# Performance work log

Measured on AMD Instinct MI355X. Metric: run time of the kernel, lower is better.

## Reference

```python
import jax, jax.numpy as jnp
import numpy as np

B, N, D, R = 4, 192, 128, 32


def _sh_l1(r):
    # e3nn l=1 real SH with 'integral' normalization: sqrt(3/4pi) * r_hat
    rh = r / (jnp.linalg.norm(r, axis=-1, keepdims=True) + 1e-12)
    return np.sqrt(3.0 / (4.0 * np.pi)).astype(np.float32) * rh


def _sh_l2(r):
    # l=2 real SH of unit vector, integral normalization, standard m=-2..2 order
    rh = r / (jnp.linalg.norm(r, axis=-1, keepdims=True) + 1e-12)
    x, y, z = rh[..., 0], rh[..., 1], rh[..., 2]
    c = np.float32(0.5 / np.sqrt(np.pi))
    s15 = np.float32(np.sqrt(15.0))
    s5h = np.float32(0.5 * np.sqrt(5.0))
    return c * jnp.stack([s15 * x * y, s15 * y * z, s5h * (3.0 * z * z - 1.0),
                          s15 * x * z, 0.5 * s15 * (x * x - y * y)], axis=-1)


def _radial(x, W1, b1, W2, b2):
    return jax.nn.silu(x @ W1 + b1) @ W2 + b2


def _forward(node_s, node_v, node_t, rbf, r_hat, mask,
             Ws1, bs1, Ws2, bs2, Wd1, bd1, Wd2, bd2,
             Wv1, bv1, Wv2, bv2, Wt1, bt1, Wt2, bt2,
             ln_g, ln_b, Wo, bo, v_scale, t_scale):
    m = mask[..., None]                      # (B,N,N,1)
    Y1 = _sh_l1(r_hat)                       # (B,N,N,3)
    Y2 = _sh_l2(r_hat)                       # (B,N,N,5)
    # scalar messages: h_j[b,i,j,d] = node_s[b,j,d]*mask; w0 also masked (mask applied twice, as in source)
    w0 = _radial(rbf, Ws1, bs1, Ws2, bs2) * m
    msg_s = jnp.einsum('bjd,bij,bijd->bid', node_s, mask, w0)
    # vector->scalar channel: source broadcasts node_v over j via unsqueeze(2), i.e. uses node_v of center i
    dot_vY = jnp.einsum('bimd,bijm->bijd', node_v, Y1)     # (B,N,N,D)
    w110 = _radial(rbf, Wd1, bd1, Wd2, bd2) * m
    msg_s_from_v = jnp.sum(dot_vY * w110, axis=2)          # (B,N,D)
    # CG tensor product 0e x SH -> irrep with per-channel radial weight, masked twice
    m2 = (mask * mask)[..., None]
    sj = node_s[:, None, :, :]                             # (B,1,N,D) -> broadcast over i
    wv = _radial(rbf, Wv1, bv1, Wv2, bv2)
    delta_v = jnp.einsum('bijd,bijm->bimd', m2 * wv * sj, Y1)   # (B,N,3,D)
    wt = _radial(rbf, Wt1, bt1, Wt2, bt2)
    delta_t = jnp.einsum('bijd,bijm->bimd', m2 * wt * sj, Y2)   # (B,N,5,D)
    # output scalar head: LayerNorm + Linear
    x = msg_s + msg_s_from_v
    mu = jnp.mean(x, axis=-1, keepdims=True)
    var = jnp.var(x, axis=-1, keepdims=True)
    delta_s = ((x - mu) / jnp.sqrt(var + 1e-5) * ln_g + ln_b) @ Wo + bo
    return delta_s, delta_v * v_scale, delta_t * t_scale


def setup_inputs() -> dict:
    ks = jax.random.split(jax.random.key(0), 16)
    g = lambda i, sh, s=1.0: jax.random.normal(ks[i], sh, jnp.float32) * s
    z = lambda: jnp.zeros((D,), jnp.float32)
    return dict(
        node_s=g(0, (B, N, D)), node_v=g(1, (B, N, 3, D)), node_t=g(2, (B, N, 5, D)),
        rbf=jax.random.uniform(ks[3], (B, N, N, R), jnp.float32),
        r_hat=g(4, (B, N, N, 3)), mask=jnp.ones((B, N, N), jnp.float32),
        Ws1=g(5, (R, D), 0.05), bs1=z(), Ws2=g(6, (D, D), 0.05), bs2=z(),
        Wd1=g(7, (R, D), 0.05), bd1=z(), Wd2=g(8, (D, D), 0.05), bd2=z(),
        Wv1=g(9, (R, D), 0.05), bv1=z(), Wv2=g(10, (D, D), 0.05), bv2=z(),
        Wt1=g(11, (R, D), 0.05), bt1=z(), Wt2=g(12, (D, D), 0.05), bt2=z(),
        ln_g=jnp.ones((D,), jnp.float32), ln_b=z(),
        Wo=g(13, (D, D), 0.05), bo=z(),
        v_scale=jnp.ones((D,), jnp.float32), t_scale=jnp.ones((D,), jnp.float32))


def reference(node_s, node_v, node_t, rbf, r_hat, mask,
              Ws1, bs1, Ws2, bs2, Wd1, bd1, Wd2, bd2,
              Wv1, bv1, Wv2, bv2, Wt1, bt1, Wt2, bt2,
              ln_g, ln_b, Wo, bo, v_scale, t_scale):
    return _forward(node_s, node_v, node_t, rbf, r_hat, mask,
                    Ws1, bs1, Ws2, bs2, Wd1, bd1, Wd2, bd2,
                    Wv1, bv1, Wv2, bv2, Wt1, bt1, Wt2, bt2,
                    ln_g, ln_b, Wo, bo, v_scale, t_scale)
```

## Files before the change

kernel.cpp:

```cpp
#include <hip/hip_runtime.h>
#include <hip/hip_bf16.h>

#define NB 192
#define DD 128
#define RR 32
#define RBS 40

typedef __attribute__((ext_vector_type(8))) short bf16x8;
typedef __attribute__((ext_vector_type(4))) float f32x4;

template<int M> struct IC { static constexpr int value = M; };

__device__ __forceinline__ unsigned short f2bf(float x) {
  union { __hip_bfloat16 h; unsigned short u; } c;
  c.h = __float2bfloat16(x);
  return c.u;
}

__global__ __launch_bounds__(256) void cg_prep(
    const float* __restrict__ Ws1, const float* __restrict__ Wd1,
    const float* __restrict__ Wv1, const float* __restrict__ Wt1,
    const float* __restrict__ Ws2, const float* __restrict__ Wd2,
    const float* __restrict__ Wv2, const float* __restrict__ Wt2,
    const float* __restrict__ bs1, const float* __restrict__ bd1,
    const float* __restrict__ bv1, const float* __restrict__ bt1,
    const float* __restrict__ bs2, const float* __restrict__ bd2,
    const float* __restrict__ bv2, const float* __restrict__ bt2,
    unsigned short* __restrict__ w1f, unsigned short* __restrict__ w2f,
    float* __restrict__ bcat1, float* __restrict__ bcat2)
{
  const float* W1s[4] = {Ws1, Wd1, Wv1, Wt1};
  const float* W2s[4] = {Ws2, Wd2, Wv2, Wt2};
  const float* B1s[4] = {bs1, bd1, bv1, bt1};
  const float* B2s[4] = {bs2, bd2, bv2, bt2};
  int t = blockIdx.x * 256 + threadIdx.x;
  if (t < 2048) {
    int lane = t & 63, f = t >> 6;
    int mlp = f >> 3, htl = f & 7;
    int g = lane >> 4, ln = lane & 15;
    const float* W = W1s[mlp];
    union { unsigned short u[8]; uint4 d; } p;
    #pragma unroll
    for (int e = 0; e < 8; ++e)
      p.u[e] = f2bf(W[(8*g + e) * DD + htl*16 + ln]);
    *(uint4*)&w1f[t * 8] = p.d;
  } else if (t < 10240) {
    int t2 = t - 2048;
    int lane = t2 & 63, f = t2 >> 6;
    int ct = f & 7, ks = (f >> 3) & 3, mlp = f >> 5;
    int g = lane >> 4, ln = lane & 15;
    const float* W = W2s[mlp];
    union { unsigned short u[8]; uint4 d; } p;
    #pragma unroll
    for (int e = 0; e < 8; ++e)
      p.u[e] = f2bf(W[(32*ks + 8*g + e) * DD + ct*16 + ln]);
    *(uint4*)&w2f[t2 * 8] = p.d;
  } else if (t < 10752) {
    int t3 = t - 10240;
    bcat1[t3] = B1s[t3 >> 7][t3 & 127];
  } else if (t < 11264) {
    int t3 = t - 10752;
    bcat2[t3] = B2s[t3 >> 7][t3 & 127];
  }
}

template<int JBLK, int MPP>
__global__ __launch_bounds__(256, 4) void cg_main(
    const float* __restrict__ node_s, const float* __restrict__ node_v,
    const float* __restrict__ rbf, const float* __restrict__ r_hat,
    const float* __restrict__ mask,
    const unsigned short* __restrict__ w1f, const unsigned short* __restrict__ w2f,
    const float* __restrict__ bcat1, const float* __restrict__ bcat2,
    float* __restrict__ ws)
{
  constexpr int NSPLIT = NB / JBLK;
  constexpr int NPASS  = 4 / MPP;
  constexpr int NT     = JBLK / 16;
  constexpr int HROW   = MPP * 128;
  constexpr int RB_B   = JBLK * RBS * 2;
  constexpr int HU_B   = JBLK * HROW * 2;
  __shared__ __align__(16) char smem[RB_B + HU_B + 9 * JBLK * 4];
  unsigned short* Rb  = (unsigned short*)smem;
  unsigned short* Hu  = (unsigned short*)(smem + RB_B);
  float*          YYf = (float*)(smem + RB_B + HU_B);

  const int tid  = threadIdx.x;
  const int bx   = blockIdx.x;
  const int bi   = bx / NSPLIT;
  const int j0   = (bx % NSPLIT) * JBLK;
  const int b    = bi / NB;
  const int wid  = tid >> 6;
  const int lane = tid & 63;
  const int g = lane >> 4, ln = lane & 15;

  auto haddr = [](int j, int hb) {
    return j * HROW + (((hb) ^ ((j & 7) << 4)) >> 1);
  };

  {
    const float4* rrow = (const float4*)(rbf + (size_t)bi * (NB * RR) + j0 * RR);
    #pragma unroll
    for (int f = tid; f < JBLK * 8; f += 256) {
      float4 v = rrow[f];
      union { unsigned short u[4]; uint2 d; } p;
      p.u[0] = f2bf(v.x); p.u[1] = f2bf(v.y); p.u[2] = f2bf(v.z); p.u[3] = f2bf(v.w);
      *(uint2*)&Rb[(f >> 3) * RBS + (f & 7) * 4] = p.d;
    }
  }
  if (tid < JBLK) {
    int jj = j0 + tid;
    const float* rh = r_hat + ((size_t)bi * NB + jj) * 3;
    float x = rh[0], y = rh[1], z = rh[2];
    float m = mask[(size_t)bi * NB + jj];
    float inv = 1.0f / (sqrtf(x*x + y*y + z*z) + 1e-12f);
    x *= inv; y *= inv; z *= inv;
    float m2 = m * m;
    YYf[0*JBLK + tid] = 0.48860252f * m * x;
    YYf[1*JBLK + tid] = 0.48860252f * m * y;
    YYf[2*JBLK + tid] = 0.48860252f * m * z;
    YYf[3*JBLK + tid] = m;
    YYf[4*JBLK + tid] = 1.09254843f * m2 * x * y;
    YYf[5*JBLK + tid] = 1.09254843f * m2 * y * z;
    YYf[6*JBLK + tid] = 0.31539157f * m2 * (3.f * z * z - 1.f);
    YYf[7*JBLK + tid] = 1.09254843f * m2 * x * z;
    YYf[8*JBLK + tid] = 0.54627422f * m2 * (x*x - y*y);
  }
  __syncthreads();

  const int c0 = wid * 32 + ln, c1 = c0 + 16;
  const float* nsb = node_s + (size_t)b * (NB * DD);
  const float* nvb = node_v + (size_t)bi * (3 * DD);
  float V00 = nvb[c0], V10 = nvb[DD + c0], V20 = nvb[2*DD + c0];
  float V01 = nvb[c1], V11 = nvb[DD + c1], V21 = nvb[2*DD + c1];

  float msgs0=0.f, msgs1=0.f, msgsv0=0.f, msgsv1=0.f;
  float dv0x=0,dv0y=0,dv0z=0, dv1x=0,dv1y=0,dv1z=0;
  float dt00=0,dt01=0,dt02=0,dt03=0,dt04=0;
  float dt10=0,dt11=0,dt12=0,dt13=0,dt14=0;

  const f32x4 zacc = {0.f, 0.f, 0.f, 0.f};

  auto do_pass = [&](auto PC) {
    constexpr int PASS = decltype(PC)::value;
    #pragma unroll
    for (int q = 0; q < MPP * 2; ++q) {
      const int idx  = wid * (MPP * 2) + q;
      const int lm   = idx >> 3;
      const int htl  = idx & 7;
      const int f    = PASS * MPP * 8 + idx;
      bf16x8 a1 = *(const bf16x8*)&w1f[(f * 64 + lane) * 8];
      float4 b1v = *(const float4*)(bcat1 + (PASS*MPP + lm) * DD + htl*16 + 4*g);
      #pragma unroll
      for (int nt = 0; nt < NT; ++nt) {
        int j = nt * 16 + ln;
        bf16x8 bb = *(const bf16x8*)&Rb[j * RBS + 8 * g];
        f32x4 h4 = __builtin_amdgcn_mfma_f32_16x16x32_bf16(a1, bb, zacc, 0, 0, 0);
        union { unsigned short u[4]; uint2 d; } hp;
        float x0 = h4[0] + b1v.x; hp.u[0] = f2bf(x0 * __builtin_amdgcn_rcpf(1.f + __expf(-x0)));
        float x1 = h4[1] + b1v.y; hp.u[1] = f2bf(x1 * __builtin_amdgcn_rcpf(1.f + __expf(-x1)));
        float x2 = h4[2] + b1v.z; hp.u[2] = f2bf(x2 * __builtin_amdgcn_rcpf(1.f + __expf(-x2)));
        float x3 = h4[3] + b1v.w; hp.u[3] = f2bf(x3 * __builtin_amdgcn_rcpf(1.f + __expf(-x3)));
        *(uint2*)&Hu[haddr(j, lm*256 + htl*32 + 8*g)] = hp.d;
      }
    }
    __syncthreads();
    auto g2 = [&](auto LC) {
      constexpr int LM   = decltype(LC)::value;
      constexpr int MODE = PASS * MPP + LM;
      float b2c0 = bcat2[MODE * DD + c0], b2c1 = bcat2[MODE * DD + c1];
      bf16x8 Bf[4][2];
      #pragma unroll
      for (int ks = 0; ks < 4; ++ks)
        #pragma unroll
        for (int t = 0; t < 2; ++t) {
          int f2 = (MODE * 4 + ks) * 8 + 2 * wid + t;
          Bf[ks][t] = *(const bf16x8*)&w2f[(f2 * 64 + lane) * 8];
        }
      #pragma unroll
      for (int mt = 0; mt < NT; ++mt) {
        int jb = mt * 16;
        f32x4 acc0 = zacc, acc1 = zacc;
        #pragma unroll
        for (int ks = 0; ks < 4; ++ks) {
          bf16x8 a = *(const bf16x8*)&Hu[haddr(jb + ln, LM*256 + ks*64 + 16*g)];
          acc0 = __builtin_amdgcn_mfma_f32_16x16x32_bf16(a, Bf[ks][0], acc0, 0, 0, 0);
          acc1 = __builtin_amdgcn_mfma_f32_16x16x32_bf16(a, Bf[ks][1], acc1, 0, 0, 0);
        }
        #pragma unroll
        for (int r = 0; r < 4; ++r) {
          int j = jb + 4*g + r;
          int jj = j0 + j;
          float w0 = acc0[r] + b2c0, w1 = acc1[r] + b2c1;
          if constexpr (MODE == 0) {
            float m = YYf[3*JBLK + j];
            float m2 = m * m;
            float ns0 = nsb[(size_t)jj*DD + c0], ns1 = nsb[(size_t)jj*DD + c1];
            msgs0 += m2 * ns0 * w0; msgs1 += m2 * ns1 * w1;
          } else if constexpr (MODE == 1) {
            float yx = YYf[0*JBLK + j], yy = YYf[1*JBLK + j], yz = YYf[2*JBLK + j];
            msgsv0 += (V00*yx + V10*yy + V20*yz) * w0;
            msgsv1 += (V01*yx + V11*yy + V21*yz) * w1;
          } else if constexpr (MODE == 2) {
            float yx = YYf[0*JBLK + j], yy = YYf[1*JBLK + j], yz = YYf[2*JBLK + j];
            float m = YYf[3*JBLK + j];
            float ns0 = nsb[(size_t)jj*DD + c0], ns1 = nsb[(size_t)jj*DD + c1];
            float t0 = m * ns0 * w0, t1 = m * ns1 * w1;
            dv0x += t0*yx; dv0y += t0*yy; dv0z += t0*yz;
            dv1x += t1*yx; dv1y += t1*yy; dv1z += t1*yz;
          } else {
            float ya = YYf[4*JBLK + j], yb = YYf[5*JBLK + j], yc = YYf[6*JBLK + j];
            float yd = YYf[7*JBLK + j], ye = YYf[8*JBLK + j];
            float ns0 = nsb[(size_t)jj*DD + c0], ns1 = nsb[(size_t)jj*DD + c1];
            float t0 = ns0 * w0, t1 = ns1 * w1;
            dt00 += t0*ya; dt01 += t0*yb; dt02 += t0*yc; dt03 += t0*yd; dt04 += t0*ye;
            dt10 += t1*ya; dt11 += t1*yb; dt12 += t1*yc; dt13 += t1*yd; dt14 += t1*ye;
          }
        }
      }
    };
    g2(IC<0>{});
    if constexpr (MPP > 1) g2(IC<1>{});
    if constexpr (MPP > 2) { g2(IC<2>{}); g2(IC<3>{}); }
    __syncthreads();
  };

  do_pass(IC<0>{});
  if constexpr (NPASS > 1) do_pass(IC<1>{});
  if constexpr (NPASS > 2) { do_pass(IC<2>{}); do_pass(IC<3>{}); }

  auto wred = [](float v) { v += __shfl_xor(v, 16); v += __shfl_xor(v, 32); return v; };
  float q0[10] = {msgs0, msgsv0, dv0x, dv0y, dv0z, dt00, dt01, dt02, dt03, dt04};
  float q1[10] = {msgs1, msgsv1, dv1x, dv1y, dv1z, dt10, dt11, dt12, dt13, dt14};
  #pragma unroll
  for (int k = 0; k < 10; ++k) { q0[k] = wred(q0[k]); q1[k] = wred(q1[k]); }
  if (g == 0) {
    float* w0 = ws + (size_t)bx * 1280;
    #pragma unroll
    for (int k = 0; k < 10; ++k) {
      w0[k*128 + c0] = q0[k];
      w0[k*128 + c1] = q1[k];
    }
  }
}

template<int NSPLIT>
__global__ __launch_bounds__(256) void cg_final(
    const float* __restrict__ ws,
    const float* __restrict__ ln_g, const float* __restrict__ ln_b,
    const float* __restrict__ Wo, const float* __restrict__ bo,
    const float* __restrict__ v_scale, const float* __restrict__ t_scale,
    float* __restrict__ out)
{
  __shared__ float Xv[128];
  __shared__ float XN[128];
  __shared__ float PS[2][128];
  __shared__ float ST[2];
  const int bi = blockIdx.x;
  const int tid = threadIdx.x;

  if (tid < 128) {
    float acc[10];
    #pragma unroll
    for (int k = 0; k < 10; ++k) acc[k] = 0.f;
    #pragma unroll
    for (int q = 0; q < NSPLIT; ++q) {
      const float* pa = ws + ((size_t)bi * NSPLIT + q) * 1280;
      #pragma unroll
      for (int k = 0; k < 10; ++k) acc[k] += pa[k*128 + tid];
    }
    float vs = v_scale[tid], ts = t_scale[tid];
    size_t vbase = 98304 + (size_t)bi * (3 * DD) + tid;
    out[vbase]        = acc[2] * vs;
    out[vbase + DD]   = acc[3] * vs;
    out[vbase + 2*DD] = acc[4] * vs;
    size_t tbase = 393216 + (size_t)bi * (5 * DD) + tid;
    out[tbase]        = acc[5] * ts;
    out[tbase + DD]   = acc[6] * ts;
    out[tbase + 2*DD] = acc[7] * ts;
    out[tbase + 3*DD] = acc[8] * ts;
    out[tbase + 4*DD] = acc[9] * ts;
    Xv[tid] = acc[0] + acc[1];
  }
  __syncthreads();
  if (tid < 64) {
    float a = Xv[tid], c = Xv[tid + 64];
    float s = a + c, ss = a*a + c*c;
    #pragma unroll
    for (int off = 32; off > 0; off >>= 1) {
      s  += __shfl_down(s, off);
      ss += __shfl_down(ss, off);
    }
    if (tid == 0) {
      float mu  = s * (1.f / 128.f);
      float var = ss * (1.f / 128.f) - mu * mu;
      ST[0] = mu; ST[1] = rsqrtf(var + 1e-5f);
    }
  }
  __syncthreads();
  if (tid < 128) XN[tid] = (Xv[tid] - ST[0]) * ST[1] * ln_g[tid] + ln_b[tid];
  __syncthreads();
  {
    int dp = tid & 127, p = tid >> 7;
    float s = 0.f;
    #pragma unroll
    for (int dd = 0; dd < 64; ++dd) {
      int d = p * 64 + dd;
      s += XN[d] * Wo[d * DD + dp];
    }
    PS[p][dp] = s;
  }
  __syncthreads();
  if (tid < 128)
    out[(size_t)bi * DD + tid] = PS[0][tid] + PS[1][tid] + bo[tid];
}

extern "C" void kernel_launch(void* const* d_in, const int* in_sizes, int n_in,
                              void* d_out, int out_size, void* d_ws, size_t ws_size,
                              hipStream_t stream) {
  (void)in_sizes; (void)n_in; (void)out_size;
  const float* node_s = (const float*)d_in[0];
  const float* node_v = (const float*)d_in[1];
  const float* rbf    = (const float*)d_in[3];
  const float* r_hat  = (const float*)d_in[4];
  const float* mask   = (const float*)d_in[5];
  const float* Ws1 = (const float*)d_in[6];  const float* bs1 = (const float*)d_in[7];
  const float* Ws2 = (const float*)d_in[8];  const float* bs2 = (const float*)d_in[9];
  const float* Wd1 = (const float*)d_in[10]; const float* bd1 = (const float*)d_in[11];
  const float* Wd2 = (const float*)d_in[12]; const float* bd2 = (const float*)d_in[13];
  const float* Wv1 = (const float*)d_in[14]; const float* bv1 = (const float*)d_in[15];
  const float* Wv2 = (const float*)d_in[16]; const float* bv2 = (const float*)d_in[17];
  const float* Wt1 = (const float*)d_in[18]; const float* bt1 = (const float*)d_in[19];
  const float* Wt2 = (const float*)d_in[20]; const float* bt2 = (const float*)d_in[21];
  const float* ln_g = (const float*)d_in[22]; const float* ln_b = (const float*)d_in[23];
  const float* Wo   = (const float*)d_in[24]; const float* bo   = (const float*)d_in[25];
  const float* v_scale = (const float*)d_in[26];
  const float* t_scale = (const float*)d_in[27];
  float* outp = (float*)d_out;

  const size_t wtail = 16384ull*2 + 65536ull*2 + 1024ull*4;
  const size_t need4 = 3072ull * 1280 * 4 + wtail;
  char* wsb = (char*)d_ws;

  bool use4 = (ws_size >= need4);
  size_t pbytes = use4 ? 3072ull * 1280 * 4 : 1536ull * 1280 * 4;
  float* partials = (float*)wsb;
  unsigned short* w1f = (unsigned short*)(wsb + pbytes);
  unsigned short* w2f = w1f + 16384;
  float* bcat1 = (float*)(w2f + 65536);
  float* bcat2 = bcat1 + 512;

  hipLaunchKernelGGL(cg_prep, dim3(44), dim3(256), 0, stream,
                     Ws1, Wd1, Wv1, Wt1, Ws2, Wd2, Wv2, Wt2,
                     bs1, bd1, bv1, bt1, bs2, bd2, bv2, bt2,
                     w1f, w2f, bcat1, bcat2);

  if (use4) {
    hipLaunchKernelGGL((cg_main<48, 2>), dim3(4 * 768), dim3(256), 0, stream,
                       node_s, node_v, rbf, r_hat, mask,
                       w1f, w2f, bcat1, bcat2, partials);
    hipLaunchKernelGGL((cg_final<4>), dim3(768), dim3(256), 0, stream,
                       partials, ln_g, ln_b, Wo, bo, v_scale, t_scale, outp);
  } else {
    hipLaunchKernelGGL((cg_main<96, 2>), dim3(2 * 768), dim3(256), 0, stream,
                       node_s, node_v, rbf, r_hat, mask,
                       w1f, w2f, bcat1, bcat2, partials);
    hipLaunchKernelGGL((cg_final<2>), dim3(768), dim3(256), 0, stream,
                       partials, ln_g, ln_b, Wo, bo, v_scale, t_scale, outp);
  }
}
```

Measured before the change: 73.55 us.

## Stage masked node_s tile in LDS as bf16 and process one MLP per pass

After: 74.08 us. No clear change (+0.7%).

```diff
diff --git a/kernel.cpp b/kernel.cpp
--- a/kernel.cpp
+++ b/kernel.cpp
@@ -5,6 +5,7 @@
 #define DD 128
 #define RR 32
 #define RBS 40
+#define SMS 136
 
 typedef __attribute__((ext_vector_type(8))) short bf16x8;
 typedef __attribute__((ext_vector_type(4))) float f32x4;
@@ -15,6 +16,10 @@
   union { __hip_bfloat16 h; unsigned short u; } c;
   c.h = __float2bfloat16(x);
   return c.u;
+}
+__device__ __forceinline__ float bf2f(unsigned short u) {
+  union { unsigned int u; float f; } c; c.u = ((unsigned int)u) << 16;
+  return c.f;
 }
 
 __global__ __launch_bounds__(256) void cg_prep(
@@ -64,7 +69,7 @@
   }
 }
 
-template<int JBLK, int MPP>
+template<int JBLK>
 __global__ __launch_bounds__(256, 4) void cg_main(
     const float* __restrict__ node_s, const float* __restrict__ node_v,
     const float* __restrict__ rbf, const float* __restrict__ r_hat,
@@ -74,15 +79,16 @@
     float* __restrict__ ws)
 {
   constexpr int NSPLIT = NB / JBLK;
-  constexpr int NPASS  = 4 / MPP;
   constexpr int NT     = JBLK / 16;
-  constexpr int HROW   = MPP * 128;
   constexpr int RB_B   = JBLK * RBS * 2;
-  constexpr int HU_B   = JBLK * HROW * 2;
-  __shared__ __align__(16) char smem[RB_B + HU_B + 9 * JBLK * 4];
+  constexpr int HU_B   = JBLK * 128 * 2;
+  constexpr int SM_B   = JBLK * SMS * 2;
+  constexpr int YY_B   = 12 * JBLK * 4;
+  __shared__ __align__(16) char smem[RB_B + HU_B + SM_B + YY_B];
   unsigned short* Rb  = (unsigned short*)smem;
   unsigned short* Hu  = (unsigned short*)(smem + RB_B);
-  float*          YYf = (float*)(smem + RB_B + HU_B);
+  unsigned short* SMu = (unsigned short*)(smem + RB_B + HU_B);
+  float*          YYf = (float*)(smem + RB_B + HU_B + SM_B);
 
   const int tid  = threadIdx.x;
   const int bx   = blockIdx.x;
@@ -94,8 +100,10 @@
   const int g = lane >> 4, ln = lane & 15;
 
   auto haddr = [](int j, int hb) {
-    return j * HROW + (((hb) ^ ((j & 7) << 4)) >> 1);
+    return j * 128 + (((hb) ^ ((j & 7) << 4)) >> 1);
   };
+
+  const float* nsb = node_s + (size_t)b * (NB * DD);
 
   {
     const float4* rrow = (const float4*)(rbf + (size_t)bi * (NB * RR) + j0 * RR);
@@ -114,21 +122,37 @@
     float m = mask[(size_t)bi * NB + jj];
     float inv = 1.0f / (sqrtf(x*x + y*y + z*z) + 1e-12f);
     x *= inv; y *= inv; z *= inv;
-    float m2 = m * m;
-    YYf[0*JBLK + tid] = 0.48860252f * m * x;
-    YYf[1*JBLK + tid] = 0.48860252f * m * y;
-    YYf[2*JBLK + tid] = 0.48860252f * m * z;
-    YYf[3*JBLK + tid] = m;
-    YYf[4*JBLK + tid] = 1.09254843f * m2 * x * y;
-    YYf[5*JBLK + tid] = 1.09254843f * m2 * y * z;
-    YYf[6*JBLK + tid] = 0.31539157f * m2 * (3.f * z * z - 1.f);
-    YYf[7*JBLK + tid] = 1.09254843f * m2 * x * z;
-    YYf[8*JBLK + tid] = 0.54627422f * m2 * (x*x - y*y);
-  }
-  __syncthreads();
+    YYf[ 0*JBLK + tid] = 0.48860252f * m * x;
+    YYf[ 1*JBLK + tid] = 0.48860252f * m * y;
+    YYf[ 2*JBLK + tid] = 0.48860252f * m * z;
+    YYf[ 3*JBLK + tid] = 0.48860252f * x;
+    YYf[ 4*JBLK + tid] = 0.48860252f * y;
+    YYf[ 5*JBLK + tid] = 0.48860252f * z;
+    YYf[ 6*JBLK + tid] = 1.09254843f * x * y;
+    YYf[ 7*JBLK + tid] = 1.09254843f * y * z;
+    YYf[ 8*JBLK + tid] = 0.31539157f * (3.f * z * z - 1.f);
+    YYf[ 9*JBLK + tid] = 1.09254843f * x * z;
+    YYf[10*JBLK + tid] = 0.54627422f * (x*x - y*y);
+    YYf[11*JBLK + tid] = m * m;
+  }
+  __syncthreads();
+
+  {
+    constexpr int ITER = (JBLK * DD) / 1024;
+    #pragma unroll
+    for (int i = 0; i < ITER; ++i) {
+      int e0 = (i * 256 + tid) * 4;
+      int j = e0 >> 7, d0 = e0 & 127;
+      float m2 = YYf[11*JBLK + j];
+      float4 v = *(const float4*)(nsb + (size_t)(j0 + j) * DD + d0);
+      union { unsigned short u[4]; uint2 dq; } p;
+      p.u[0] = f2bf(m2*v.x); p.u[1] = f2bf(m2*v.y);
+      p.u[2] = f2bf(m2*v.z); p.u[3] = f2bf(m2*v.w);
+      *(uint2*)&SMu[j * SMS + d0] = p.dq;
+    }
+  }
 
   const int c0 = wid * 32 + ln, c1 = c0 + 16;
-  const float* nsb = node_s + (size_t)b * (NB * DD);
   const float* nvb = node_v + (size_t)bi * (3 * DD);
   float V00 = nvb[c0], V10 = nvb[DD + c0], V20 = nvb[2*DD + c0];
   float V01 = nvb[c1], V11 = nvb[DD + c1], V21 = nvb[2*DD + c1];
@@ -141,15 +165,22 @@
   const f32x4 zacc = {0.f, 0.f, 0.f, 0.f};
 
   auto do_pass = [&](auto PC) {
-    constexpr int PASS = decltype(PC)::value;
-    #pragma unroll
-    for (int q = 0; q < MPP * 2; ++q) {
-      const int idx  = wid * (MPP * 2) + q;
-      const int lm   = idx >> 3;
-      const int htl  = idx & 7;
-      const int f    = PASS * MPP * 8 + idx;
+    constexpr int MODE = decltype(PC)::value;
+    bf16x8 Bf[4][2];
+    #pragma unroll
+    for (int ks = 0; ks < 4; ++ks)
+      #pragma unroll
+      for (int t = 0; t < 2; ++t) {
+        int f2 = (MODE * 4 + ks) * 8 + 2 * wid + t;
+        Bf[ks][t] = *(const bf16x8*)&w2f[(f2 * 64 + lane) * 8];
+      }
+    float b2c0 = bcat2[MODE * DD + c0], b2c1 = bcat2[MODE * DD + c1];
+    #pragma unroll
+    for (int q = 0; q < 2; ++q) {
+      const int htl = wid * 2 + q;
+      const int f   = MODE * 8 + htl;
       bf16x8 a1 = *(const bf16x8*)&w1f[(f * 64 + lane) * 8];
-      float4 b1v = *(const float4*)(bcat1 + (PASS*MPP + lm) * DD + htl*16 + 4*g);
+      float4 b1v = *(const float4*)(bcat1 + MODE * DD + htl*16 + 4*g);
       #pragma unroll
       for (int nt = 0; nt < NT; ++nt) {
         int j = nt * 16 + ln;
@@ -160,73 +191,54 @@
         float x1 = h4[1] + b1v.y; hp.u[1] = f2bf(x1 * __builtin_amdgcn_rcpf(1.f + __expf(-x1)));
         float x2 = h4[2] + b1v.z; hp.u[2] = f2bf(x2 * __builtin_amdgcn_rcpf(1.f + __expf(-x2)));
         float x3 = h4[3] + b1v.w; hp.u[3] = f2bf(x3 * __builtin_amdgcn_rcpf(1.f + __expf(-x3)));
-        *(uint2*)&Hu[haddr(j, lm*256 + htl*32 + 8*g)] = hp.d;
+        *(uint2*)&Hu[haddr(j, htl*32 + 8*g)] = hp.d;
       }
     }
     __syncthreads();
-    auto g2 = [&](auto LC) {
-      constexpr int LM   = decltype(LC)::value;
-      constexpr int MODE = PASS * MPP + LM;
-      float b2c0 = bcat2[MODE * DD + c0], b2c1 = bcat2[MODE * DD + c1];
-      bf16x8 Bf[4][2];
-      #pragma unroll
-      for (int ks = 0; ks < 4; ++ks)
-        #pragma unroll
-        for (int t = 0; t < 2; ++t) {
-          int f2 = (MODE * 4 + ks) * 8 + 2 * wid + t;
-          Bf[ks][t] = *(const bf16x8*)&w2f[(f2 * 64 + lane) * 8];
-        }
-      #pragma unroll
-      for (int mt = 0; mt < NT; ++mt) {
-        int jb = mt * 16;
-        f32x4 acc0 = zacc, acc1 = zacc;
-        #pragma unroll
-        for (int ks = 0; ks < 4; ++ks) {
-          bf16x8 a = *(const bf16x8*)&Hu[haddr(jb + ln, LM*256 + ks*64 + 16*g)];
-          acc0 = __builtin_amdgcn_mfma_f32_16x16x32_bf16(a, Bf[ks][0], acc0, 0, 0, 0);
-          acc1 = __builtin_amdgcn_mfma_f32_16x16x32_bf16(a, Bf[ks][1], acc1, 0, 0, 0);
-        }
-        #pragma unroll
-        for (int r = 0; r < 4; ++r) {
-          int j = jb + 4*g + r;
-          int jj = j0 + j;
-          float w0 = acc0[r] + b2c0, w1 = acc1[r] + b2c1;
-          if constexpr (MODE == 0) {
-            float m = YYf[3*JBLK + j];
-            float m2 = m * m;
-            float ns0 = nsb[(size_t)jj*DD + c0], ns1 = nsb[(size_t)jj*DD + c1];
-            msgs0 += m2 * ns0 * w0; msgs1 += m2 * ns1 * w1;
-          } else if constexpr (MODE == 1) {
-            float yx = YYf[0*JBLK + j], yy = YYf[1*JBLK + j], yz = YYf[2*JBLK + j];
-            msgsv0 += (V00*yx + V10*yy + V20*yz) * w0;
-            msgsv1 += (V01*yx + V11*yy + V21*yz) * w1;
-          } else if constexpr (MODE == 2) {
-            float yx = YYf[0*JBLK + j], yy = YYf[1*JBLK + j], yz = YYf[2*JBLK + j];
-            float m = YYf[3*JBLK + j];
-            float ns0 = nsb[(size_t)jj*DD + c0], ns1 = nsb[(size_t)jj*DD + c1];
-            float t0 = m * ns0 * w0, t1 = m * ns1 * w1;
-            dv0x += t0*yx; dv0y += t0*yy; dv0z += t0*yz;
-            dv1x += t1*yx; dv1y += t1*yy; dv1z += t1*yz;
-          } else {
-            float ya = YYf[4*JBLK + j], yb = YYf[5*JBLK + j], yc = YYf[6*JBLK + j];
-            float yd = YYf[7*JBLK + j], ye = YYf[8*JBLK + j];
-            float ns0 = nsb[(size_t)jj*DD + c0], ns1 = nsb[(size_t)jj*DD + c1];
-            float t0 = ns0 * w0, t1 = ns1 * w1;
-            dt00 += t0*ya; dt01 += t0*yb; dt02 += t0*yc; dt03 += t0*yd; dt04 += t0*ye;
-            dt10 += t1*ya; dt11 += t1*yb; dt12 += t1*yc; dt13 += t1*yd; dt14 += t1*ye;
-          }
+    #pragma unroll
+    for (int mt = 0; mt < NT; ++mt) {
+      int jb = mt * 16;
+      f32x4 acc0 = zacc, acc1 = zacc;
+      #pragma unroll
+      for (int ks = 0; ks < 4; ++ks) {
+        bf16x8 a = *(const bf16x8*)&Hu[haddr(jb + ln, ks*64 + 16*g)];
+        acc0 = __builtin_amdgcn_mfma_f32_16x16x32_bf16(a, Bf[ks][0], acc0, 0, 0, 0);
+        acc1 = __builtin_amdgcn_mfma_f32_16x16x32_bf16(a, Bf[ks][1], acc1, 0, 0, 0);
+      }
+      #pragma unroll
+      for (int r = 0; r < 4; ++r) {
+        int j = jb + 4*g + r;
+        float w0 = acc0[r] + b2c0, w1 = acc1[r] + b2c1;
+        if constexpr (MODE == 0) {
+          float s0 = bf2f(SMu[j*SMS + c0]), s1 = bf2f(SMu[j*SMS + c1]);
+          msgs0 += s0 * w0; msgs1 += s1 * w1;
+        } else if constexpr (MODE == 1) {
+          float yx = YYf[0*JBLK + j], yy = YYf[1*JBLK + j], yz = YYf[2*JBLK + j];
+          msgsv0 += (V00*yx + V10*yy + V20*yz) * w0;
+          msgsv1 += (V01*yx + V11*yy + V21*yz) * w1;
+        } else if constexpr (MODE == 2) {
+          float yx = YYf[3*JBLK + j], yy = YYf[4*JBLK + j], yz = YYf[5*JBLK + j];
+          float s0 = bf2f(SMu[j*SMS + c0]), s1 = bf2f(SMu[j*SMS + c1]);
+          float t0 = s0 * w0, t1 = s1 * w1;
+          dv0x += t0*yx; dv0y += t0*yy; dv0z += t0*yz;
+          dv1x += t1*yx; dv1y += t1*yy; dv1z += t1*yz;
+        } else {
+          float ya = YYf[6*JBLK + j], yb = YYf[7*JBLK + j], yc = YYf[8*JBLK + j];
+          float yd = YYf[9*JBLK + j], ye = YYf[10*JBLK + j];
+          float s0 = bf2f(SMu[j*SMS + c0]), s1 = bf2f(SMu[j*SMS + c1]);
+          float t0 = s0 * w0, t1 = s1 * w1;
+          dt00 += t0*ya; dt01 += t0*yb; dt02 += t0*yc; dt03 += t0*yd; dt04 += t0*ye;
+          dt10 += t1*ya; dt11 += t1*yb; dt12 += t1*yc; dt13 += t1*yd; dt14 += t1*ye;
         }
       }
-    };
-    g2(IC<0>{});
-    if constexpr (MPP > 1) g2(IC<1>{});
-    if constexpr (MPP > 2) { g2(IC<2>{}); g2(IC<3>{}); }
+    }
     __syncthreads();
   };
 
   do_pass(IC<0>{});
-  if constexpr (NPASS > 1) do_pass(IC<1>{});
-  if constexpr (NPASS > 2) { do_pass(IC<2>{}); do_pass(IC<3>{}); }
+  do_pass(IC<1>{});
+  do_pass(IC<2>{});
+  do_pass(IC<3>{});
 
   auto wred = [](float v) { v += __shfl_xor(v, 16); v += __shfl_xor(v, 32); return v; };
   float q0[10] = {msgs0, msgsv0, dv0x, dv0y, dv0z, dt00, dt01, dt02, dt03, dt04};
@@ -355,13 +367,13 @@
                      w1f, w2f, bcat1, bcat2);
 
   if (use4) {
-    hipLaunchKernelGGL((cg_main<48, 2>), dim3(4 * 768), dim3(256), 0, stream,
+    hipLaunchKernelGGL((cg_main<48>), dim3(4 * 768), dim3(256), 0, stream,
                        node_s, node_v, rbf, r_hat, mask,
                        w1f, w2f, bcat1, bcat2, partials);
     hipLaunchKernelGGL((cg_final<4>), dim3(768), dim3(256), 0, stream,
                        partials, ln_g, ln_b, Wo, bo, v_scale, t_scale, outp);
   } else {
-    hipLaunchKernelGGL((cg_main<96, 2>), dim3(2 * 768), dim3(256), 0, stream,
+    hipLaunchKernelGGL((cg_main<96>), dim3(2 * 768), dim3(256), 0, stream,
                        node_s, node_v, rbf, r_hat, mask,
                        w1f, w2f, bcat1, bcat2, partials);
     hipLaunchKernelGGL((cg_final<2>), dim3(768), dim3(256), 0, stream,
```
